# Kernel optimization log

Hardware: AMD Instinct MI355X
Metric: run time of the kernel (lower is better)

The kernel has to match this reference:

```python
import jax, jax.numpy as jnp
import numpy as np

SQRT2 = np.sqrt(2.0)
# pywt orthonormal Haar analysis filters
H0 = np.array([1.0, 1.0]) / SQRT2   # dec_lo
H1 = np.array([-1.0, 1.0]) / SQRT2  # dec_hi


def make_A(N, h0=H0, h1=H1):
    """NxN analysis filter-bank matrix: top N/2 rows lowpass (stride 2,
    circular), bottom N/2 rows highpass. Matches
    get_A_matrix_dwt_analysisFB_unit for an orthonormal wavelet."""
    L = len(h0)
    A = np.zeros((N, N), dtype=np.float32)
    for i in range(N // 2):
        for k in range(L):
            c = (2 * i + k) % N
            A[i, c] += h0[k]
            A[N // 2 + i, c] += h1[k]
    return jnp.asarray(A)


def setup_inputs() -> dict:
    key = jax.random.key(0)
    B, N, C = 2, 128, 4
    x = jax.random.normal(key, (B, N, N, N, C), dtype=jnp.float32)
    A = make_A(N)
    return {"x": x, "A": A}


def reference(x, A):
    # Separable 3D DWT: apply A along each spatial axis.
    # (vectorized over channels; original loops per channel with identical A)
    y = jnp.einsum('ai,nijkc->najkc', A, x)   # axis 1
    y = jnp.einsum('bj,najkc->nabkc', A, y)   # axis 2
    y = jnp.einsum('dk,nabkc->nabdc', A, y)   # axis 3
    # Subband split (faithful to original slicing, incl. HLH == HHH slice)
    mid = y.shape[2] // 2
    LLL = y[:, :mid, :mid, :mid, :]
    LLH = y[:, mid:, :mid, :mid, :]
    LHL = y[:, :mid, mid:, :mid, :]
    LHH = y[:, mid:, mid:, :mid, :]
    HLL = y[:, :mid, :mid, mid:, :]
    HLH = y[:, mid:, mid:, mid:, :]
    HHL = y[:, :mid, mid:, mid:, :]
    HHH = y[:, mid:, mid:, mid:, :]
    return jnp.concatenate([LLL, LLH, LHL, LHH, HLL, HLH, HHL, HHH], axis=-1)
```

## Files before the change

### kernel.cpp

```cpp
#include <hip/hip_runtime.h>


__device__ __forceinline__ float4 lin(float c0, const float4& u, float c1, const float4& v) {
    return make_float4(fmaf(c0, u.x, c1 * v.x),
                       fmaf(c0, u.y, c1 * v.y),
                       fmaf(c0, u.z, c1 * v.z),
                       fmaf(c0, u.w, c1 * v.w));
}

__global__ __launch_bounds__(256) void dwt3d_haar_kernel(
        const float* __restrict__ x,
        const float* __restrict__ A,
        float* __restrict__ out) {
    const int t = blockIdx.x * blockDim.x + threadIdx.x;
    const int d = t & 63;
    const int b = (t >> 6) & 63;
    const int a = (t >> 12) & 63;
    const int n = t >> 18;

    const float h00 = A[0];
    const float h01 = A[1];
    const float h10 = A[64 * 128 + 0];
    const float h11 = A[64 * 128 + 1];

    const float4* __restrict__ x4 = reinterpret_cast<const float4*>(x);
    float4* __restrict__ o4 = reinterpret_cast<float4*>(out);

    const int ib = n * 2097152 + a * 32768 + b * 256 + d * 2;

    float4 p[2][2][2];
    #pragma unroll
    for (int i = 0; i < 2; ++i) {
        #pragma unroll
        for (int j = 0; j < 2; ++j) {
            const int o = ib + i * 16384 + j * 128;
            p[i][j][0] = x4[o];
            p[i][j][1] = x4[o + 1];
        }
    }

    float4 A0[2][2], A1[2][2];
    #pragma unroll
    for (int j = 0; j < 2; ++j) {
        #pragma unroll
        for (int k = 0; k < 2; ++k) {
            A0[j][k] = lin(h00, p[0][j][k], h01, p[1][j][k]);
            A1[j][k] = lin(h10, p[0][j][k], h11, p[1][j][k]);
        }
    }

    float4 B00[2], B01[2], B10[2], B11[2];
    #pragma unroll
    for (int k = 0; k < 2; ++k) {
        B00[k] = lin(h00, A0[0][k], h01, A0[1][k]);
        B01[k] = lin(h10, A0[0][k], h11, A0[1][k]);
        B10[k] = lin(h00, A1[0][k], h01, A1[1][k]);
        B11[k] = lin(h10, A1[0][k], h11, A1[1][k]);
    }

    const float4 v000 = lin(h00, B00[0], h01, B00[1]);
    const float4 v001 = lin(h10, B00[0], h11, B00[1]);
    const float4 v010 = lin(h00, B01[0], h01, B01[1]);
    const float4 v011 = lin(h10, B01[0], h11, B01[1]);
    const float4 v100 = lin(h00, B10[0], h01, B10[1]);
    const float4 v110 = lin(h00, B11[0], h01, B11[1]);
    const float4 v111 = lin(h10, B11[0], h11, B11[1]);

    const int ob = n * 2097152 + a * 32768 + b * 512 + d * 8;
    o4[ob + 0] = v000;
    o4[ob + 1] = v100;
    o4[ob + 2] = v010;
    o4[ob + 3] = v110;
    o4[ob + 4] = v001;
    o4[ob + 5] = v111;
    o4[ob + 6] = v011;
    o4[ob + 7] = v111;
}

extern "C" void kernel_launch(void* const* d_in, const int* in_sizes, int n_in,
                              void* d_out, int out_size, void* d_ws, size_t ws_size,
                              hipStream_t stream) {
    const float* x = (const float*)d_in[0];
    const float* A = (const float*)d_in[1];
    float* out = (float*)d_out;

    const int total = 2 * 64 * 64 * 64;
    const int block = 256;
    const int grid = total / block;
    hipLaunchKernelGGL(dwt3d_haar_kernel, dim3(grid), dim3(block), 0, stream,
                       x, A, out);
}
```

Baseline: 123.5 us.

## Split each Haar 2x2x2 block across 8 lanes with warp shuffle butterflies

Each thread now loads one float4 of a 2x2x2 input block and the three separable Haar stages are computed by exchanging values between lanes via xor shuffles, so each thread writes exactly one output vector. This gives 8x more threads, fewer registers per thread and fully contiguous per-thread output stores, aiming for better memory-level parallelism. It adds cross-lane shuffle traffic and a special case to reproduce the duplicated HHH subband.

Measured after the change: 109.5 us, median of 2. -11.3%, faster.

```diff
diff --git a/kernel.cpp b/kernel.cpp
--- a/kernel.cpp
+++ b/kernel.cpp
@@ -8,73 +8,65 @@
                        fmaf(c0, u.w, c1 * v.w));
 }
 
-__global__ __launch_bounds__(256) void dwt3d_haar_kernel(
+__device__ __forceinline__ float4 shfl_xor4(const float4& v, int mask) {
+    return make_float4(__shfl_xor(v.x, mask),
+                       __shfl_xor(v.y, mask),
+                       __shfl_xor(v.z, mask),
+                       __shfl_xor(v.w, mask));
+}
+
+__global__ __launch_bounds__(256) void dwt3d_haar_bfly(
         const float* __restrict__ x,
         const float* __restrict__ A,
         float* __restrict__ out) {
     const int t = blockIdx.x * blockDim.x + threadIdx.x;
-    const int d = t & 63;
-    const int b = (t >> 6) & 63;
-    const int a = (t >> 12) & 63;
-    const int n = t >> 18;
+    const int c = t & 7;
+    const int d = (t >> 3) & 63;
+    const int b = (t >> 9) & 63;
+    const int a = (t >> 15) & 63;
+    const int n = t >> 21;
 
     const float h00 = A[0];
     const float h01 = A[1];
     const float h10 = A[64 * 128 + 0];
     const float h11 = A[64 * 128 + 1];
 
+    const int i0 = c & 1;
+    const int j0 = (c >> 1) & 1;
+    const int k0 = (c >> 2) & 1;
+
     const float4* __restrict__ x4 = reinterpret_cast<const float4*>(x);
-    float4* __restrict__ o4 = reinterpret_cast<float4*>(out);
+    const int xi = n * 2097152 + a * 32768 + b * 256 + d * 2
+                 + i0 * 16384 + j0 * 128 + k0;
+    float4 v = x4[xi];
 
-    const int ib = n * 2097152 + a * 32768 + b * 256 + d * 2;
-
-    float4 p[2][2][2];
-    #pragma unroll
-    for (int i = 0; i < 2; ++i) {
-        #pragma unroll
-        for (int j = 0; j < 2; ++j) {
-            const int o = ib + i * 16384 + j * 128;
-            p[i][j][0] = x4[o];
-            p[i][j][1] = x4[o + 1];
-        }
+    {
+        const float4 w = shfl_xor4(v, 1);
+        const float4 p0 = i0 ? w : v;
+        const float4 p1 = i0 ? v : w;
+        const float c0 = i0 ? h10 : h00;
+        const float c1 = i0 ? h11 : h01;
+        v = lin(c0, p0, c1, p1);
+    }
+    {
+        const float4 w = shfl_xor4(v, 4);
+        const float4 p0 = k0 ? w : v;
+        const float4 p1 = k0 ? v : w;
+        const float c0 = k0 ? h10 : h00;
+        const float c1 = k0 ? h11 : h01;
+        v = lin(c0, p0, c1, p1);
+    }
+    {
+        const float4 w = shfl_xor4(v, 2);
+        const float4 p0 = j0 ? w : v;
+        const float4 p1 = j0 ? v : w;
+        const int sb = j0 | (c == 5 ? 1 : 0);
+        const float c0 = sb ? h10 : h00;
+        const float c1 = sb ? h11 : h01;
+        v = lin(c0, p0, c1, p1);
     }
 
-    float4 A0[2][2], A1[2][2];
-    #pragma unroll
-    for (int j = 0; j < 2; ++j) {
-        #pragma unroll
-        for (int k = 0; k < 2; ++k) {
-            A0[j][k] = lin(h00, p[0][j][k], h01, p[1][j][k]);
-            A1[j][k] = lin(h10, p[0][j][k], h11, p[1][j][k]);
-        }
-    }
-
-    float4 B00[2], B01[2], B10[2], B11[2];
-    #pragma unroll
-    for (int k = 0; k < 2; ++k) {
-        B00[k] = lin(h00, A0[0][k], h01, A0[1][k]);
-        B01[k] = lin(h10, A0[0][k], h11, A0[1][k]);
-        B10[k] = lin(h00, A1[0][k], h01, A1[1][k]);
-        B11[k] = lin(h10, A1[0][k], h11, A1[1][k]);
-    }
-
-    const float4 v000 = lin(h00, B00[0], h01, B00[1]);
-    const float4 v001 = lin(h10, B00[0], h11, B00[1]);
-    const float4 v010 = lin(h00, B01[0], h01, B01[1]);
-    const float4 v011 = lin(h10, B01[0], h11, B01[1]);
-    const float4 v100 = lin(h00, B10[0], h01, B10[1]);
-    const float4 v110 = lin(h00, B11[0], h01, B11[1]);
-    const float4 v111 = lin(h10, B11[0], h11, B11[1]);
-
-    const int ob = n * 2097152 + a * 32768 + b * 512 + d * 8;
-    o4[ob + 0] = v000;
-    o4[ob + 1] = v100;
-    o4[ob + 2] = v010;
-    o4[ob + 3] = v110;
-    o4[ob + 4] = v001;
-    o4[ob + 5] = v111;
-    o4[ob + 6] = v011;
-    o4[ob + 7] = v111;
+    reinterpret_cast<float4*>(out)[t] = v;
 }
 
 extern "C" void kernel_launch(void* const* d_in, const int* in_sizes, int n_in,
@@ -84,9 +76,9 @@
     const float* A = (const float*)d_in[1];
     float* out = (float*)d_out;
 
-    const int total = 2 * 64 * 64 * 64;
+    const int total = 2 * 64 * 64 * 64 * 8;
     const int block = 256;
     const int grid = total / block;
-    hipLaunchKernelGGL(dwt3d_haar_kernel, dim3(grid), dim3(block), 0, stream,
+    hipLaunchKernelGGL(dwt3d_haar_bfly, dim3(grid), dim3(block), 0, stream,
                        x, A, out);
 }
```
